# Optimization experiments

Measured on AMD Instinct MI355X. Metric: run time of the kernel, lower is better.

## Reference

```python
import jax, jax.numpy as jnp
import numpy as np

KH = KW = 3
K = KH * KW
STRIDE = 1
PAD = 1
DIL = 1
DG = 1  # deformable groups


def conv2d(x, w, b):
    out = jax.lax.conv_general_dilated(
        x, w, window_strides=(STRIDE, STRIDE),
        padding=[(PAD, PAD), (PAD, PAD)], rhs_dilation=(DIL, DIL),
        dimension_numbers=('NCHW', 'OIHW', 'NCHW'))
    return out + b[None, :, None, None]


def deform_conv2d(x, offset, mask, w, b):
    """DCNv2: bilinear sample at predicted offsets, modulate by mask, GEMM with w."""
    B, Cin, H, W = x.shape
    Ho, Wo = offset.shape[2], offset.shape[3]
    cpg = Cin // DG
    # torchvision layout: channel 2*(g*K+k) = dy, 2*(g*K+k)+1 = dx
    off = offset.reshape(B, DG, K, 2, Ho, Wo)
    off_y, off_x = off[:, :, :, 0], off[:, :, :, 1]  # [B,DG,K,Ho,Wo]
    m = mask.reshape(B, DG, K, Ho, Wo)
    ky = jnp.repeat(jnp.arange(KH), KW) * DIL          # [K] kernel row offsets
    kx = jnp.tile(jnp.arange(KW), KH) * DIL            # [K] kernel col offsets
    hh = jnp.arange(Ho) * STRIDE - PAD
    ww = jnp.arange(Wo) * STRIDE - PAD
    py = off_y + ky[None, None, :, None, None] + hh[None, None, None, :, None]
    px = off_x + kx[None, None, :, None, None] + ww[None, None, None, None, :]
    y0 = jnp.floor(py); x0 = jnp.floor(px)
    wy = py - y0; wx = px - x0
    x_g = x.reshape(B, DG, cpg, H * W)

    def gather(yc, xc):  # zero-padded bilinear corner fetch
        valid = ((yc >= 0) & (yc < H) & (xc >= 0) & (xc < W)).astype(x.dtype)
        yi = jnp.clip(yc, 0, H - 1).astype(jnp.int32)
        xi = jnp.clip(xc, 0, W - 1).astype(jnp.int32)
        idx = (yi * W + xi).reshape(B, DG, 1, K * Ho * Wo)
        v = jnp.take_along_axis(x_g, jnp.broadcast_to(idx, (B, DG, cpg, K * Ho * Wo)), axis=3)
        return v.reshape(B, DG, cpg, K, Ho, Wo) * valid[:, :, None]

    v00 = gather(y0, x0)
    v01 = gather(y0, x0 + 1)
    v10 = gather(y0 + 1, x0)
    v11 = gather(y0 + 1, x0 + 1)
    wy_b = wy[:, :, None]; wx_b = wx[:, :, None]  # broadcast over cpg
    sampled = (v00 * (1 - wy_b) * (1 - wx_b) + v01 * (1 - wy_b) * wx_b
               + v10 * wy_b * (1 - wx_b) + v11 * wy_b * wx_b)
    sampled = (sampled * m[:, :, None]).reshape(B, Cin, K, Ho, Wo)
    Cout = w.shape[0]
    out = jnp.einsum('bckhw,ock->bohw', sampled, w.reshape(Cout, Cin, K))
    return out + b[None, :, None, None]


def setup_inputs() -> dict:
    key = jax.random.key(0)
    k1, k2, k3, k4 = jax.random.split(key, 4)
    B, Cin, Cout, H, W = 8, 128, 128, 64, 64
    omc = DG * 3 * K  # 2*K offsets + K mask channels = 27
    x = jax.random.normal(k1, (B, Cin, H, W), dtype=jnp.float32)
    # small offset-conv weights -> modest predicted offsets (mimics near-zero init)
    w_off = jax.random.normal(k2, (omc, Cin, KH, KW), dtype=jnp.float32) * 0.01
    b_off = jnp.zeros((omc,), dtype=jnp.float32)
    w_def = jax.random.normal(k3, (Cout, Cin, KH, KW), dtype=jnp.float32) * (1.0 / np.sqrt(Cin * K))
    b_def = jax.random.normal(k4, (Cout,), dtype=jnp.float32) * 0.01
    return {"x": x, "w_off": w_off, "b_off": b_off, "w_def": w_def, "b_def": b_def}


def reference(x, w_off, b_off, w_def, b_def):
    out = conv2d(x, w_off, b_off)
    oc = DG * 2 * K
    offset = out[:, :oc]
    mask = jax.nn.sigmoid(out[:, oc:])
    return deform_conv2d(x, offset, mask, w_def, b_def)
```

## Files before the change

### kernel.cpp

```cpp
#include <hip/hip_runtime.h>
#include <math.h>

typedef _Float16 f16;
typedef __attribute__((ext_vector_type(2))) _Float16 f16x2;
typedef __attribute__((ext_vector_type(4))) _Float16 f16x4;
typedef __attribute__((ext_vector_type(8))) _Float16 f16x8;
typedef __attribute__((ext_vector_type(4))) float f32x4;

#define NBATCH 8
#define WSA_ELE 36864
#define WSB_ELE 147456
#define PREP_BLOCKS 720
#define OFF_WSB  73728
#define OFF_XT   368640
#define OFF_OFFM 8757248

__device__ __forceinline__ void gload_lds16(const f16* gsrc, f16* ldst) {
  __builtin_amdgcn_global_load_lds(
      (const __attribute__((address_space(1))) unsigned int*)gsrc,
      (__attribute__((address_space(3))) unsigned int*)ldst, 16, 0, 0);
}

__global__ __launch_bounds__(256) void prep_kernel(const float* __restrict__ x,
                                                   const float* __restrict__ w_off,
                                                   const float* __restrict__ w_def,
                                                   f16* __restrict__ wsA,
                                                   f16* __restrict__ wsB,
                                                   f16* __restrict__ xt) {
  __shared__ f16 s_t[128 * 66];
  const int bid = blockIdx.x;
  const int t = threadIdx.x;
  if (bid < PREP_BLOCKS) {
    int i = bid * 256 + t;
    if (i < WSA_ELE) {
      int j = i & 7, lane = (i >> 3) & 63, fm = i >> 9;
      int ch = fm >> 1, mt = fm & 1;
      int row = mt * 16 + (lane & 15);
      int kidx = ch * 32 + (lane >> 4) * 8 + j;
      int k = kidx >> 7, cc = kidx & 127;
      float v = (row < 27) ? w_off[row * 1152 + cc * 9 + k] : 0.0f;
      wsA[i] = (f16)v;
    } else {
      int e = i - WSA_ELE;
      int j = e & 7, lane = (e >> 3) & 63, fm = e >> 9;
      int ch = fm >> 3, mt = fm & 7;
      int row = mt * 16 + (lane & 15);
      int kidx = ch * 32 + (lane >> 4) * 8 + j;
      int k = kidx >> 7, cc = kidx & 127;
      wsB[e] = (f16)w_def[row * 1152 + cc * 9 + k];
    }
  } else {
    const int bb = bid - PREP_BLOCKS;
    const int b = bb >> 6;
    const int pos0 = (bb & 63) << 6;
    const float* xb = x + ((size_t)b << 19);
    for (int i = t; i < 8192; i += 256) {
      int c = i >> 6, p = i & 63;
      s_t[c * 66 + p] = (f16)xb[c * 4096 + pos0 + p];
    }
    __syncthreads();
    f16* xtb = xt + ((size_t)b << 19);
    for (int i = t; i < 4096; i += 256) {
      int p = i >> 6, c2 = (i & 63) * 2;
      unsigned v0 = *(const unsigned short*)&s_t[c2 * 66 + p];
      unsigned v1 = *(const unsigned short*)&s_t[(c2 + 1) * 66 + p];
      *(unsigned*)&xtb[(size_t)(pos0 + p) * 128 + c2] = v0 | (v1 << 16);
    }
  }
}

__global__ __launch_bounds__(256) void offset_conv_kernel(const f16* __restrict__ xt,
                                                          const f16* __restrict__ wsA,
                                                          const float* __restrict__ b_off,
                                                          float* __restrict__ offm) {
  const int t = threadIdx.x;
  const int b = blockIdx.x >> 6, ho = blockIdx.x & 63;
  const int lane = t & 63, wid = t >> 6;
  const int q = lane >> 4, li = lane & 15;
  const int px = (wid << 4) + li;
  const char* xtb = (const char*)xt + ((size_t)b << 20);

  f32x4 acc0 = {0.f, 0.f, 0.f, 0.f}, acc1 = {0.f, 0.f, 0.f, 0.f};

  for (int k = 0; k < 9; ++k) {
    const int ky = k / 3, kx = k - ky * 3;
    const int y = ho + ky - 1;
    const int xx = px + kx - 1;
    const bool valid = ((unsigned)y < 64u) && ((unsigned)xx < 64u);
    const int pos = min(max(y, 0), 63) * 64 + min(max(xx, 0), 63);
    const int voff = pos * 256 + q * 16;
    #pragma unroll
    for (int c4 = 0; c4 < 4; ++c4) {
      union { uint4 u; f16x8 v; } bu;
      bu.u = *(const uint4*)(xtb + voff + c4 * 64);
      if (!valid) { bu.u.x = 0u; bu.u.y = 0u; bu.u.z = 0u; bu.u.w = 0u; }
      const int ch = k * 4 + c4;
      f16x8 a0 = *(const f16x8*)&wsA[(ch * 2    ) * 512 + lane * 8];
      f16x8 a1 = *(const f16x8*)&wsA[(ch * 2 + 1) * 512 + lane * 8];
      acc0 = __builtin_amdgcn_mfma_f32_16x16x32_f16(a0, bu.v, acc0, 0, 0, 0);
      acc1 = __builtin_amdgcn_mfma_f32_16x16x32_f16(a1, bu.v, acc1, 0, 0, 0);
    }
  }

  float* om = offm + (size_t)b * 27 * 4096 + ho * 64 + px;
  #pragma unroll
  for (int mt = 0; mt < 2; ++mt) {
    f32x4 a = mt ? acc1 : acc0;
    #pragma unroll
    for (int r = 0; r < 4; ++r) {
      int oc = mt * 16 + q * 4 + r;
      if (oc < 27) {
        float v = a[r] + b_off[oc];
        if (oc >= 18) v = 1.0f / (1.0f + __expf(-v));
        om[oc * 4096] = v;
      }
    }
  }
}

__global__ __launch_bounds__(256, 5) void dcn_kernel(const f16* __restrict__ xt,
                                                     const f16* __restrict__ wsB,
                                                     const float* __restrict__ offm,
                                                     const float* __restrict__ b_def,
                                                     float* __restrict__ out) {
  __shared__ ushort4 s_pos[576];
  __shared__ f16x4   s_wth[576];
  __shared__ __align__(16) f16 s_a[8192];
  const int t = threadIdx.x;
  const int b = blockIdx.x >> 6, ho = blockIdx.x & 63;
  const int lane = t & 63, wid = t >> 6;
  const int q = lane >> 4, li = lane & 15;
  const int px0 = wid << 4;
  const char* xtb = (const char*)xt + ((size_t)b << 20);

  const float* ob = offm + (size_t)b * 27 * 4096 + ho * 64;
  for (int f = t; f < 576; f += 256) {
    int k = f >> 6, p = f & 63;
    int ky = k / 3, kx = k - ky * 3;
    float oy = ob[(2 * k    ) * 4096 + p];
    float ox = ob[(2 * k + 1) * 4096 + p];
    float m  = ob[(18 + k   ) * 4096 + p];
    float py  = oy + (float)(ho + ky - 1);
    float pxf = ox + (float)(p + kx - 1);
    float y0f = floorf(py), x0f = floorf(pxf);
    float wy = py - y0f, wx = pxf - x0f;
    int y0 = (int)y0f, x0 = (int)x0f;
    int y1 = y0 + 1, x1 = x0 + 1;
    bool y0v = (unsigned)y0 < 64u, y1v = (unsigned)y1 < 64u;
    bool x0v = (unsigned)x0 < 64u, x1v = (unsigned)x1 < 64u;
    int y0c = min(max(y0, 0), 63), y1c = min(max(y1, 0), 63);
    int x0c = min(max(x0, 0), 63), x1c = min(max(x1, 0), 63);
    ushort4 p4;
    p4.x = (unsigned short)(y0c * 64 + x0c);
    p4.y = (unsigned short)(y0c * 64 + x1c);
    p4.z = (unsigned short)(y1c * 64 + x0c);
    p4.w = (unsigned short)(y1c * 64 + x1c);
    f16x4 wh;
    wh[0] = (f16)((y0v && x0v) ? (1.f - wy) * (1.f - wx) * m : 0.f);
    wh[1] = (f16)((y0v && x1v) ? (1.f - wy) * wx         * m : 0.f);
    wh[2] = (f16)((y1v && x0v) ? wy         * (1.f - wx) * m : 0.f);
    wh[3] = (f16)((y1v && x1v) ? wy         * wx         * m : 0.f);
    s_pos[f] = p4;
    s_wth[f] = wh;
  }

  f32x4 acc[8];
  #pragma unroll
  for (int mt = 0; mt < 8; ++mt) acc[mt] = (f32x4){0.f, 0.f, 0.f, 0.f};

  for (int c4g = 0; c4g < 36; ++c4g) {
    const int k = c4g >> 2, c4 = c4g & 3, sub = c4g & 1;
    if (sub == 0) {
      __syncthreads();
      const f16* src = wsB + c4g * 4096 + wid * 2048 + lane * 8;
      f16* dst = &s_a[wid * 2048];
      gload_lds16(src,        dst);
      gload_lds16(src +  512, dst +  512);
      gload_lds16(src + 1024, dst + 1024);
      gload_lds16(src + 1536, dst + 1536);
      __syncthreads();
    }
    const int e = k * 64 + px0 + li;
    const ushort4 p4 = s_pos[e];
    const f16x4   w4 = s_wth[e];
    const unsigned cb = (unsigned)(c4 * 64 + q * 16);
    union { uint4 u; f16x2 h[4]; } d0, d1, d2, d3;
    d0.u = *(const uint4*)(xtb + (((unsigned)p4.x << 8) + cb));
    d1.u = *(const uint4*)(xtb + (((unsigned)p4.y << 8) + cb));
    d2.u = *(const uint4*)(xtb + (((unsigned)p4.z << 8) + cb));
    d3.u = *(const uint4*)(xtb + (((unsigned)p4.w << 8) + cb));
    const f16x2 wp0 = {w4[0], w4[0]}, wp1 = {w4[1], w4[1]};
    const f16x2 wp2 = {w4[2], w4[2]}, wp3 = {w4[3], w4[3]};
    union { f16x2 h[4]; f16x8 v; } bf;
    #pragma unroll
    for (int i = 0; i < 4; ++i) {
      f16x2 s = d0.h[i] * wp0;
      s = s + d1.h[i] * wp1;
      s = s + d2.h[i] * wp2;
      s = s + d3.h[i] * wp3;
      bf.h[i] = s;
    }
    const f16* ab = &s_a[sub * 4096];
    #pragma unroll
    for (int mt = 0; mt < 8; ++mt) {
      f16x8 a = *(const f16x8*)&ab[(mt * 64 + lane) * 8];
      acc[mt] = __builtin_amdgcn_mfma_f32_16x16x32_f16(a, bf.v, acc[mt], 0, 0, 0);
    }
  }

  float* o = out + (size_t)b * 128 * 4096 + ho * 64 + px0 + li;
  #pragma unroll
  for (int mt = 0; mt < 8; ++mt) {
    #pragma unroll
    for (int r = 0; r < 4; ++r) {
      int oc = mt * 16 + q * 4 + r;
      o[oc * 4096] = acc[mt][r] + b_def[oc];
    }
  }
}

extern "C" void kernel_launch(void* const* d_in, const int* in_sizes, int n_in,
                              void* d_out, int out_size, void* d_ws, size_t ws_size,
                              hipStream_t stream) {
  const float* x     = (const float*)d_in[0];
  const float* w_off = (const float*)d_in[1];
  const float* b_off = (const float*)d_in[2];
  const float* w_def = (const float*)d_in[3];
  const float* b_def = (const float*)d_in[4];
  float* out = (float*)d_out;

  f16*   wsA  = (f16*)d_ws;
  f16*   wsB  = (f16*)((char*)d_ws + OFF_WSB);
  f16*   xt   = (f16*)((char*)d_ws + OFF_XT);
  float* offm = (float*)((char*)d_ws + OFF_OFFM);

  prep_kernel<<<dim3(PREP_BLOCKS + NBATCH * 64), dim3(256), 0, stream>>>(x, w_off, w_def, wsA, wsB, xt);
  offset_conv_kernel<<<dim3(NBATCH * 64), dim3(256), 0, stream>>>(xt, wsA, b_off, offm);
  dcn_kernel<<<dim3(NBATCH * 64), dim3(256), 0, stream>>>(xt, wsB, offm, b_def, out);
}
```

Measured before the change: 136.0 us.

## Fuse offset conv into DCN kernel and split K across two blocks with atomics

Merges the offset/mask convolution into the deformable conv kernel, keeping offsets in shared memory instead of round-tripping through a global buffer, and removes one launch. The 9-tap reduction is split into two halves across twice as many blocks, which accumulate into an output pre-initialised with bias by the prep kernel using atomicAdd. Each half block recomputes the full offset conv, which duplicates that work. The atomics add output traffic and make float summation order nondeterministic.

```diff
diff --git a/kernel.cpp b/kernel.cpp
--- a/kernel.cpp
+++ b/kernel.cpp
@@ -10,10 +10,11 @@
 #define NBATCH 8
 #define WSA_ELE 36864
 #define WSB_ELE 147456
-#define PREP_BLOCKS 720
+#define WPREP_BLOCKS 720
+#define XPREP_BLOCKS 512
+#define OPREP_BLOCKS 1024
 #define OFF_WSB  73728
 #define OFF_XT   368640
-#define OFF_OFFM 8757248
 
 __device__ __forceinline__ void gload_lds16(const f16* gsrc, f16* ldst) {
   __builtin_amdgcn_global_load_lds(
@@ -24,13 +25,15 @@
 __global__ __launch_bounds__(256) void prep_kernel(const float* __restrict__ x,
                                                    const float* __restrict__ w_off,
                                                    const float* __restrict__ w_def,
+                                                   const float* __restrict__ b_def,
                                                    f16* __restrict__ wsA,
                                                    f16* __restrict__ wsB,
-                                                   f16* __restrict__ xt) {
+                                                   f16* __restrict__ xt,
+                                                   float* __restrict__ out) {
   __shared__ f16 s_t[128 * 66];
   const int bid = blockIdx.x;
   const int t = threadIdx.x;
-  if (bid < PREP_BLOCKS) {
+  if (bid < WPREP_BLOCKS) {
     int i = bid * 256 + t;
     if (i < WSA_ELE) {
       int j = i & 7, lane = (i >> 3) & 63, fm = i >> 9;
@@ -49,8 +52,8 @@
       int k = kidx >> 7, cc = kidx & 127;
       wsB[e] = (f16)w_def[row * 1152 + cc * 9 + k];
     }
-  } else {
-    const int bb = bid - PREP_BLOCKS;
+  } else if (bid < WPREP_BLOCKS + XPREP_BLOCKS) {
+    const int bb = bid - WPREP_BLOCKS;
     const int b = bb >> 6;
     const int pos0 = (bb & 63) << 6;
     const float* xb = x + ((size_t)b << 19);
@@ -66,22 +69,34 @@
       unsigned v1 = *(const unsigned short*)&s_t[(c2 + 1) * 66 + p];
       *(unsigned*)&xtb[(size_t)(pos0 + p) * 128 + c2] = v0 | (v1 << 16);
     }
-  }
-}
-
-__global__ __launch_bounds__(256) void offset_conv_kernel(const f16* __restrict__ xt,
-                                                          const f16* __restrict__ wsA,
-                                                          const float* __restrict__ b_off,
-                                                          float* __restrict__ offm) {
-  const int t = threadIdx.x;
-  const int b = blockIdx.x >> 6, ho = blockIdx.x & 63;
-  const int lane = t & 63, wid = t >> 6;
+  } else {
+    const int ob = bid - (WPREP_BLOCKS + XPREP_BLOCKS);
+    const float bv = b_def[ob & 127];
+    float4 v = {bv, bv, bv, bv};
+    float4* p = (float4*)(out + (size_t)ob * 4096 + t * 16);
+    p[0] = v; p[1] = v; p[2] = v; p[3] = v;
+  }
+}
+
+__global__ __launch_bounds__(256, 4) void dcn_fused_kernel(const f16* __restrict__ xt,
+                                                           const f16* __restrict__ wsA,
+                                                           const f16* __restrict__ wsB,
+                                                           const float* __restrict__ b_off,
+                                                           const float* __restrict__ b_def,
+                                                           float* __restrict__ out) {
+  __shared__ __align__(16) f16 s_a[8192];
+  __shared__ ushort4 s_pos[5 * 64];
+  __shared__ f16x4   s_wth[5 * 64];
+  const int bid = blockIdx.x;
+  const int half = bid >> 9;
+  const int b = (bid >> 6) & 7, ho = bid & 63;
+  const int t = threadIdx.x, lane = t & 63, wid = t >> 6;
   const int q = lane >> 4, li = lane & 15;
   const int px = (wid << 4) + li;
   const char* xtb = (const char*)xt + ((size_t)b << 20);
-
-  f32x4 acc0 = {0.f, 0.f, 0.f, 0.f}, acc1 = {0.f, 0.f, 0.f, 0.f};
-
+  float* s_off = (float*)s_a;
+
+  f32x4 oa0 = {0.f, 0.f, 0.f, 0.f}, oa1 = {0.f, 0.f, 0.f, 0.f};
   for (int k = 0; k < 9; ++k) {
     const int ky = k / 3, kx = k - ky * 3;
     const int y = ho + ky - 1;
@@ -97,49 +112,33 @@
       const int ch = k * 4 + c4;
       f16x8 a0 = *(const f16x8*)&wsA[(ch * 2    ) * 512 + lane * 8];
       f16x8 a1 = *(const f16x8*)&wsA[(ch * 2 + 1) * 512 + lane * 8];
-      acc0 = __builtin_amdgcn_mfma_f32_16x16x32_f16(a0, bu.v, acc0, 0, 0, 0);
-      acc1 = __builtin_amdgcn_mfma_f32_16x16x32_f16(a1, bu.v, acc1, 0, 0, 0);
-    }
-  }
-
-  float* om = offm + (size_t)b * 27 * 4096 + ho * 64 + px;
+      oa0 = __builtin_amdgcn_mfma_f32_16x16x32_f16(a0, bu.v, oa0, 0, 0, 0);
+      oa1 = __builtin_amdgcn_mfma_f32_16x16x32_f16(a1, bu.v, oa1, 0, 0, 0);
+    }
+  }
   #pragma unroll
   for (int mt = 0; mt < 2; ++mt) {
-    f32x4 a = mt ? acc1 : acc0;
+    f32x4 a = mt ? oa1 : oa0;
     #pragma unroll
     for (int r = 0; r < 4; ++r) {
       int oc = mt * 16 + q * 4 + r;
       if (oc < 27) {
         float v = a[r] + b_off[oc];
         if (oc >= 18) v = 1.0f / (1.0f + __expf(-v));
-        om[oc * 4096] = v;
+        s_off[oc * 65 + px] = v;
       }
     }
   }
-}
-
-__global__ __launch_bounds__(256, 5) void dcn_kernel(const f16* __restrict__ xt,
-                                                     const f16* __restrict__ wsB,
-                                                     const float* __restrict__ offm,
-                                                     const float* __restrict__ b_def,
-                                                     float* __restrict__ out) {
-  __shared__ ushort4 s_pos[576];
-  __shared__ f16x4   s_wth[576];
-  __shared__ __align__(16) f16 s_a[8192];
-  const int t = threadIdx.x;
-  const int b = blockIdx.x >> 6, ho = blockIdx.x & 63;
-  const int lane = t & 63, wid = t >> 6;
-  const int q = lane >> 4, li = lane & 15;
-  const int px0 = wid << 4;
-  const char* xtb = (const char*)xt + ((size_t)b << 20);
-
-  const float* ob = offm + (size_t)b * 27 * 4096 + ho * 64;
-  for (int f = t; f < 576; f += 256) {
-    int k = f >> 6, p = f & 63;
+  __syncthreads();
+
+  const int klo = half * 4;
+  for (int f = t; f < 320; f += 256) {
+    int kk = f >> 6, p = f & 63;
+    int k = klo + kk;
     int ky = k / 3, kx = k - ky * 3;
-    float oy = ob[(2 * k    ) * 4096 + p];
-    float ox = ob[(2 * k + 1) * 4096 + p];
-    float m  = ob[(18 + k   ) * 4096 + p];
+    float oy = s_off[(2 * k    ) * 65 + p];
+    float ox = s_off[(2 * k + 1) * 65 + p];
+    float m  = s_off[(18 + k   ) * 65 + p];
     float py  = oy + (float)(ho + ky - 1);
     float pxf = ox + (float)(p + kx - 1);
     float y0f = floorf(py), x0f = floorf(pxf);
@@ -168,8 +167,10 @@
   #pragma unroll
   for (int mt = 0; mt < 8; ++mt) acc[mt] = (f32x4){0.f, 0.f, 0.f, 0.f};
 
-  for (int c4g = 0; c4g < 36; ++c4g) {
-    const int k = c4g >> 2, c4 = c4g & 3, sub = c4g & 1;
+  const int cg0 = half * 18;
+  for (int s = 0; s < 18; ++s) {
+    const int c4g = cg0 + s;
+    const int k = c4g >> 2, c4 = c4g & 3, sub = s & 1;
     if (sub == 0) {
       __syncthreads();
       const f16* src = wsB + c4g * 4096 + wid * 2048 + lane * 8;
@@ -180,7 +181,7 @@
       gload_lds16(src + 1536, dst + 1536);
       __syncthreads();
     }
-    const int e = k * 64 + px0 + li;
+    const int e = (k - klo) * 64 + px;
     const ushort4 p4 = s_pos[e];
     const f16x4   w4 = s_wth[e];
     const unsigned cb = (unsigned)(c4 * 64 + q * 16);
@@ -194,11 +195,11 @@
     union { f16x2 h[4]; f16x8 v; } bf;
     #pragma unroll
     for (int i = 0; i < 4; ++i) {
-      f16x2 s = d0.h[i] * wp0;
-      s = s + d1.h[i] * wp1;
-      s = s + d2.h[i] * wp2;
-      s = s + d3.h[i] * wp3;
-      bf.h[i] = s;
+      f16x2 sm = d0.h[i] * wp0;
+      sm = sm + d1.h[i] * wp1;
+      sm = sm + d2.h[i] * wp2;
+      sm = sm + d3.h[i] * wp3;
+      bf.h[i] = sm;
     }
     const f16* ab = &s_a[sub * 4096];
     #pragma unroll
@@ -208,13 +209,13 @@
     }
   }
 
-  float* o = out + (size_t)b * 128 * 4096 + ho * 64 + px0 + li;
+  float* o = out + ((size_t)b << 19) + ho * 64 + px;
   #pragma unroll
   for (int mt = 0; mt < 8; ++mt) {
     #pragma unroll
     for (int r = 0; r < 4; ++r) {
       int oc = mt * 16 + q * 4 + r;
-      o[oc * 4096] = acc[mt][r] + b_def[oc];
+      atomicAdd(o + oc * 4096, acc[mt][r]);
     }
   }
 }
@@ -229,12 +230,12 @@
   const float* b_def = (const float*)d_in[4];
   float* out = (float*)d_out;
 
-  f16*   wsA  = (f16*)d_ws;
-  f16*   wsB  = (f16*)((char*)d_ws + OFF_WSB);
-  f16*   xt   = (f16*)((char*)d_ws + OFF_XT);
-  float* offm = (float*)((char*)d_ws + OFF_OFFM);
-
-  prep_kernel<<<dim3(PREP_BLOCKS + NBATCH * 64), dim3(256), 0, stream>>>(x, w_off, w_def, wsA, wsB, xt);
-  offset_conv_kernel<<<dim3(NBATCH * 64), dim3(256), 0, stream>>>(xt, wsA, b_off, offm);
-  dcn_kernel<<<dim3(NBATCH * 64), dim3(256), 0, stream>>>(xt, wsB, offm, b_def, out);
-}
+  f16* wsA = (f16*)d_ws;
+  f16* wsB = (f16*)((char*)d_ws + OFF_WSB);
+  f16* xt  = (f16*)((char*)d_ws + OFF_XT);
+
+  prep_kernel<<<dim3(WPREP_BLOCKS + XPREP_BLOCKS + OPREP_BLOCKS), dim3(256), 0, stream>>>(
+      x, w_off, w_def, b_def, wsA, wsB, xt, out);
+  dcn_fused_kernel<<<dim3(2 * NBATCH * 64), dim3(256), 0, stream>>>(
+      xt, wsA, wsB, b_off, b_def, out);
+}
```

New measurement: 158.5 us. 16.5% more time.
